# Optimization experiments

Measured on AMD Instinct MI355X. Metric: run time of the kernel, lower is better.

## Reference

```python
import jax, jax.numpy as jnp
import numpy as np
from functools import partial

MAX_SPAN_WIDTH = 8


def setup_inputs() -> dict:
    key = jax.random.key(0)
    ks = jax.random.split(key, 8)
    B, S, H = 4, 256, 256
    NE, D = 50000, 256  # entity_embedding_dim == hidden_size
    inp = {
        "embeddings": jax.random.normal(ks[0], (B, S, H), jnp.float32),          # BERT outputs[0]
        "entity_table": jax.random.normal(ks[1], (NE, D), jnp.float32) * 0.02,   # nn.Embedding weight
        "span_W": jax.random.normal(ks[2], (2 * H + 1, H), jnp.float32) * 0.02,  # span_embedding Linear
        "span_b": jax.random.normal(ks[3], (H,), jnp.float32) * 0.02,
        "gcn_W1": jax.random.normal(ks[4], (D, H), jnp.float32) * 0.02,
        "gcn_b1": jax.random.normal(ks[5], (H,), jnp.float32) * 0.02,
        "gcn_W2": jax.random.normal(ks[6], (H, H), jnp.float32) * 0.02,
        "gcn_b2": jax.random.normal(ks[7], (H,), jnp.float32) * 0.02,
        "k": 8,
    }
    return inp


def _star_adj_norm(k, dtype):
    # k-node star graph (node 0 hub) with self-loops, symmetric GCN normalization
    A = jnp.zeros((k, k), dtype).at[0, 1:].set(1.0).at[1:, 0].set(1.0) + jnp.eye(k, dtype=dtype)
    deg = A.sum(axis=1)
    return A / jnp.sqrt(deg[:, None] * deg[None, :])


def reference(embeddings, entity_table, span_W, span_b, gcn_W1, gcn_b1, gcn_W2, gcn_b2, k):
    B, S, H = embeddings.shape
    Wmax = MAX_SPAN_WIDTH
    dtype = embeddings.dtype

    # token_inputs: CLS embedding per example
    cls = embeddings[:, 0, :]  # [B, H]

    # Vectorized ragged span max-pool: running max over widths 1..Wmax.
    # span_max[w, b, s, :] = max(embeddings[b, s : s+w+1, :])
    neg_inf = jnp.array(-jnp.inf, dtype)
    maxes = []
    cur = embeddings
    maxes.append(cur)
    for w in range(1, Wmax):
        shifted = jnp.concatenate(
            [embeddings[:, w:, :], jnp.full((B, w, H), neg_inf, dtype)], axis=1)
        cur = jnp.maximum(cur, shifted)  # -inf pad => out-of-range positions ignored
        maxes.append(cur)
    span_max = jnp.stack(maxes, axis=0)  # [Wmax, B, S, H]

    # concat(max-pool, CLS, span width) -> span_embedding Linear
    cls_b = jnp.broadcast_to(cls[None, :, None, :], (Wmax, B, S, H))
    width_feat = jnp.broadcast_to(
        jnp.arange(1, Wmax + 1, dtype=dtype)[:, None, None, None], (Wmax, B, S, 1))
    span_inputs = jnp.concatenate([span_max, cls_b, width_feat], axis=-1)  # [Wmax,B,S,2H+1]
    span_inputs = span_inputs.reshape(Wmax * B * S, 2 * H + 1)             # [N, 2H+1]
    span_repr = span_inputs @ span_W + span_b                              # [N, H]

    # build_subgraph: top-k similar entities per span (memory-bound similarity + top-k)
    sims = span_repr @ entity_table.T          # [N, NE]  ~1.6GB intermediate
    _, topk_idx = jax.lax.top_k(sims, k)       # [N, k]
    node_x = entity_table[topk_idx]            # gather -> [N, k, D]

    # 2-layer GCN on the fixed star subgraph (gather-linear-scatter equivalent)
    A_norm = _star_adj_norm(k, dtype)          # [k, k]
    h = jax.nn.relu(jnp.einsum('ij,njd,dh->nih', A_norm, node_x, gcn_W1) + gcn_b1)
    subgraph_out = jnp.einsum('ij,njd,dh->nih', A_norm, h, gcn_W2) + gcn_b2  # [N, k, H]

    return cls, span_repr, subgraph_out
```

## Files before the change

### kernel.cpp

```cpp
#include <hip/hip_runtime.h>

typedef unsigned short u16;
typedef unsigned int   u32;
typedef unsigned long long u64;
typedef short bf16x8 __attribute__((ext_vector_type(8)));
typedef float f32x4  __attribute__((ext_vector_type(4)));

#define INF_F __builtin_inff()

__device__ __forceinline__ u16 f2bf(float f) {
  u32 u = __float_as_uint(f);
  return (u16)((u + 0x7FFFu + ((u >> 16) & 1u)) >> 16);
}

__device__ __forceinline__ u32 sortf(float f) {
  u32 u = __float_as_uint(f);
  return u ^ ((u32)((int)u >> 31) | 0x80000000u);
}
__device__ __forceinline__ float unsortf(u32 s) {
  u32 u = s ^ ((s & 0x80000000u) ? 0x80000000u : 0xFFFFFFFFu);
  return __uint_as_float(u);
}
__device__ __forceinline__ u64 sx64(u64 v, int m) {
  u32 lo = __shfl_xor((u32)v, m);
  u32 hi = __shfl_xor((u32)(v >> 32), m);
  return ((u64)hi << 32) | lo;
}

__global__ __launch_bounds__(256) void k0_cvt(
    const float* __restrict__ src, u16* __restrict__ dst, int n4) {
  int id = blockIdx.x * 256 + threadIdx.x;
  if (id >= n4) return;
  float4 v = ((const float4*)src)[id];
  ((ushort4*)dst)[id] = make_ushort4(f2bf(v.x), f2bf(v.y), f2bf(v.z), f2bf(v.w));
}

__global__ __launch_bounds__(256) void k1_span(
    const float* __restrict__ emb, const float* __restrict__ Wsp,
    const float* __restrict__ bsp,
    float* __restrict__ out0, float* __restrict__ out1,
    u16* __restrict__ spanbf) {
  __shared__ float SM[8][256];
  __shared__ float CLS[256];
  const int bid = blockIdx.x;
  const int b = bid >> 8, s = bid & 255;
  const int t = threadIdx.x;
  const float* eb = emb + (size_t)b * 65536;

  CLS[t] = eb[t];
  if (s == 0) out0[b * 256 + t] = eb[t];

  float m = eb[s * 256 + t];
  SM[0][t] = m;
  #pragma unroll
  for (int w = 1; w < 8; ++w) {
    if (s + w < 256) m = fmaxf(m, eb[(s + w) * 256 + t]);
    SM[w][t] = m;
  }
  __syncthreads();

  float cc = 0.f;
  for (int k = 0; k < 256; k += 4) {
    float4 cq = *(const float4*)&CLS[k];
    cc += cq.x * Wsp[(size_t)(256 + k + 0) * 256 + t];
    cc += cq.y * Wsp[(size_t)(256 + k + 1) * 256 + t];
    cc += cq.z * Wsp[(size_t)(256 + k + 2) * 256 + t];
    cc += cq.w * Wsp[(size_t)(256 + k + 3) * 256 + t];
  }
  float acc[8];
  const float base = bsp[t] + cc;
  #pragma unroll
  for (int w = 0; w < 8; ++w) acc[w] = base;

  for (int k = 0; k < 256; k += 4) {
    float w0 = Wsp[(size_t)(k + 0) * 256 + t];
    float w1 = Wsp[(size_t)(k + 1) * 256 + t];
    float w2 = Wsp[(size_t)(k + 2) * 256 + t];
    float w3 = Wsp[(size_t)(k + 3) * 256 + t];
    #pragma unroll
    for (int w = 0; w < 8; ++w) {
      float4 smq = *(const float4*)&SM[w][k];
      acc[w] += smq.x * w0; acc[w] += smq.y * w1;
      acc[w] += smq.z * w2; acc[w] += smq.w * w3;
    }
  }
  const float wm = Wsp[(size_t)512 * 256 + t];
  #pragma unroll
  for (int w = 0; w < 8; ++w) {
    float val = acc[w] + (float)(w + 1) * wm;
    size_t idx = ((size_t)w * 1024 + bid) * 256 + t;
    out1[idx] = val;
    spanbf[idx] = f2bf(val);
  }
}

__global__ __launch_bounds__(256) void k2_mfma(
    const u16* __restrict__ spanbf, const u16* __restrict__ entbf, int ne,
    float* __restrict__ Rpv, int* __restrict__ Rpi) {
  __shared__ u32 Elds[8192];
  __shared__ u64 Q[4][16][17];
  const int t = threadIdx.x, lane = t & 63, wv = t >> 6;
  const int m = lane & 15, q = lane >> 4, q4 = q * 4;
  const int rg = blockIdx.x & 63, p = blockIdx.x >> 6;
  const int psz = (ne + 7) >> 3;
  const int e_start = p * psz;
  const int e_end = min(ne, e_start + psz);
  const int rowbase = rg * 128 + wv * 32;
  const u64 gm = 0xFFFFull << (q * 16);
  const u64 lanelow = (lane == 63) ? 0x7FFFFFFFFFFFFFFFull
                                   : ((1ull << (lane + 1)) - 1) >> 1;
  const u64 gml = gm & lanelow;
  const int row = lane & 15;

  const u64 KINIT = ((u64)sortf(-INF_F) << 32);
  u64 slot0[4], slot1[4];
  #pragma unroll
  for (int s = 0; s < 4; ++s) { slot0[s] = KINIT; slot1[s] = KINIT; }
  float myth0 = -INF_F, myth1 = -INF_F;
  float th0[4], th1[4];
  #pragma unroll
  for (int r = 0; r < 4; ++r) { th0[r] = -INF_F; th1[r] = -INF_F; }

  bf16x8 a0[8], a1[8];
  #pragma unroll
  for (int s = 0; s < 8; ++s) {
    a0[s] = *(const bf16x8*)(spanbf + (size_t)(rowbase + m) * 256 + s * 32 + q * 8);
    a1[s] = *(const bf16x8*)(spanbf + (size_t)(rowbase + 16 + m) * 256 + s * 32 + q * 8);
  }

  uint4 stg[8];
  auto load_stage = [&](int tile) {
    const int ebs = e_start + (tile << 6);
    #pragma unroll
    for (int i = 0; i < 8; ++i) {
      int id = t + 256 * i; int e = id >> 5, qq = id & 31;
      int ge = ebs + e;
      uint4 v = make_uint4(0u, 0u, 0u, 0u);
      if (ge < e_end) v = *(const uint4*)((const char*)entbf + (size_t)ge * 512 + qq * 16);
      stg[i] = v;
    }
  };
  auto write_stage = [&]() {
    #pragma unroll
    for (int i = 0; i < 8; ++i) {
      int id = t + 256 * i; int e = id >> 5, qq = id & 31;
      *(uint4*)((char*)Elds + (((e << 5) | (qq ^ (e & 31))) << 4)) = stg[i];
    }
  };

  const int ntiles = (e_end - e_start + 63) >> 6;
  load_stage(0);

  for (int tile = 0; tile < ntiles; ++tile) {
    const int eb = e_start + (tile << 6);
    __syncthreads();
    write_stage();
    if (tile + 1 < ntiles) load_stage(tile + 1);
    __syncthreads();

    for (int c = 0; c < 4; ++c) {
      f32x4 acc0 = {0.f, 0.f, 0.f, 0.f}, acc1 = {0.f, 0.f, 0.f, 0.f};
      const int el = c * 16 + m, sw = el & 31, bc = el << 5;
      #pragma unroll
      for (int s = 0; s < 8; ++s) {
        int qq = s * 4 + q;
        bf16x8 bfr = *(const bf16x8*)((const char*)Elds + ((bc | (qq ^ sw)) << 4));
        acc0 = __builtin_amdgcn_mfma_f32_16x16x32_bf16(a0[s], bfr, acc0, 0, 0, 0);
        acc1 = __builtin_amdgcn_mfma_f32_16x16x32_bf16(a1[s], bfr, acc1, 0, 0, 0);
      }
      const int gent = eb + c * 16 + m;
      const bool valid = gent < e_end;

      auto produce = [&](const f32x4& av, const float* th, u64* M) {
        #pragma unroll
        for (int r = 0; r < 4; ++r) {
          bool hr = valid && (av[r] > th[r]);
          u64 br = __ballot(hr);
          M[r] = br;
          if (hr) {
            int pos = (int)__popcll(br & gml);
            Q[wv][q4 + r][pos] = ((u64)sortf(av[r]) << 32) | (u32)(~(u32)gent);
          }
        }
      };
      auto drain = [&](const u64* M, u64* slot, float& myth) {
        if (!(M[0] | M[1] | M[2] | M[3])) return;
        u64 msk = (row & 2) ? ((row & 1) ? M[3] : M[2])
                            : ((row & 1) ? M[1] : M[0]);
        int cnt = (int)__popcll((msk >> ((row >> 2) << 4)) & 0xFFFFull);
        int cmax = cnt;
        #pragma unroll
        for (int o = 1; o < 16; o <<= 1)
          cmax = max(cmax, __shfl_xor(cmax, o));
        for (int j = 0; j < cmax; ++j) {
          u64 cand = Q[wv][row][j];
          if (j >= cnt) cand = 0;
          u64 m01 = slot[0] < slot[1] ? slot[0] : slot[1];
          u64 m23 = slot[2] < slot[3] ? slot[2] : slot[3];
          u64 lmin = m01 < m23 ? m01 : m23;
          u64 g = sx64(lmin, 16); if (g < lmin) lmin = g;
          g = sx64(lmin, 32); u64 gmin = (g < lmin) ? g : lmin;
          bool ins = cand > gmin;
          #pragma unroll
          for (int s2 = 0; s2 < 4; ++s2)
            if (ins && slot[s2] == gmin) slot[s2] = cand;
        }
        u64 m01 = slot[0] < slot[1] ? slot[0] : slot[1];
        u64 m23 = slot[2] < slot[3] ? slot[2] : slot[3];
        u64 lmin = m01 < m23 ? m01 : m23;
        u64 g = sx64(lmin, 16); if (g < lmin) lmin = g;
        g = sx64(lmin, 32); if (g < lmin) lmin = g;
        myth = unsortf((u32)(lmin >> 32));
      };

      u64 M0[4], M1[4];
      produce(acc0, th0, M0);
      drain(M0, slot0, myth0);
      produce(acc1, th1, M1);
      drain(M1, slot1, myth1);
      if (M0[0] | M0[1] | M0[2] | M0[3]) {
        #pragma unroll
        for (int r = 0; r < 4; ++r) th0[r] = __shfl(myth0, q4 + r);
      }
      if (M1[0] | M1[1] | M1[2] | M1[3]) {
        #pragma unroll
        for (int r = 0; r < 4; ++r) th1[r] = __shfl(myth1, q4 + r);
      }
    }
  }

  {
    const int sg = lane >> 4;
    const int r0 = rowbase + row, r1 = rowbase + 16 + row;
    #pragma unroll
    for (int s = 0; s < 4; ++s) {
      u64 e0 = slot0[s], e1 = slot1[s];
      int col = p * 16 + sg * 4 + s;
      Rpv[(size_t)r0 * 128 + col] = unsortf((u32)(e0 >> 32));
      Rpi[(size_t)r0 * 128 + col] = (int)(~(u32)e0);
      Rpv[(size_t)r1 * 128 + col] = unsortf((u32)(e1 >> 32));
      Rpi[(size_t)r1 * 128 + col] = (int)(~(u32)e1);
    }
  }
}

__global__ __launch_bounds__(256) void k2_merge(
    const float* __restrict__ Rpv, const int* __restrict__ Rpi,
    int* __restrict__ Ridx) {
  const int t = threadIdx.x, lane = t & 63, wv = t >> 6;
  const int row = blockIdx.x * 4 + wv;
  const float va = Rpv[(size_t)row * 128 + lane];
  const int   ea = Rpi[(size_t)row * 128 + lane];
  const float vb = Rpv[(size_t)row * 128 + 64 + lane];
  const int   eb = Rpi[(size_t)row * 128 + 64 + lane];
  int ca = 0, cb = 0;
  for (int i = 0; i < 64; ++i) {
    float ov = __shfl(va, i); int oi = __shfl(ea, i);
    ca += (ov > va || (ov == va && oi < ea));
    cb += (ov > vb || (ov == vb && oi < eb));
  }
  for (int i = 0; i < 64; ++i) {
    float ov = __shfl(vb, i); int oi = __shfl(eb, i);
    ca += (ov > va || (ov == va && oi < ea));
    cb += (ov > vb || (ov == vb && oi < eb));
  }
  if (ca < 16) Ridx[(size_t)row * 16 + ca] = ea;
  if (cb < 16) Ridx[(size_t)row * 16 + cb] = eb;
}

__global__ __launch_bounds__(256, 3) void k3_gcn(
    const float* __restrict__ out1, const float* __restrict__ ent,
    const int* __restrict__ Ridx,
    const float* __restrict__ W1, const float* __restrict__ b1,
    const float* __restrict__ W2, const float* __restrict__ b2,
    float* __restrict__ out2, int ne) {
  __shared__ __align__(16) char UN[34560];
  __shared__ __align__(16) u16 Abf[32][272];
  __shared__ int cidx[4][16];
  __shared__ int chos[4][8];
  const int t = threadIdx.x;
  const int lane = t & 63, wv = t >> 6;
  const int m = lane & 15, q = lane >> 4;
  const int n0 = blockIdx.x * 4;

  {
    float  (*SPR)[256] = (float (*)[256])UN;
    double (*dpart)[4] = (double (*)[4])(UN + 4096);
    double (*sims)[16] = (double (*)[16])(UN + 6144);
    #pragma unroll
    for (int g = 0; g < 4; ++g)
      SPR[g][t] = out1[(size_t)(n0 + g) * 256 + t];
    if (t < 64) {
      int g = t >> 4, j = t & 15;
      int c = Ridx[(size_t)(n0 + g) * 16 + j];
      if ((unsigned)c >= (unsigned)ne) c = 0;
      cidx[g][j] = c;
    }
    __syncthreads();

    {
      const int pr = t >> 2, sub = t & 3;
      const int g = pr >> 4, j = pr & 15;
      const float* er = ent + (size_t)cidx[g][j] * 256 + sub * 64;
      const float* sr = &SPR[g][sub * 64];
      double s = 0.0;
      #pragma unroll
      for (int i = 0; i < 64; i += 4) {
        float4 e4 = *(const float4*)&er[i];
        float4 s4 = *(const float4*)&sr[i];
        s += (double)e4.x * (double)s4.x;
        s += (double)e4.y * (double)s4.y;
        s += (double)e4.z * (double)s4.z;
        s += (double)e4.w * (double)s4.w;
      }
      dpart[pr][sub] = s;
    }
    __syncthreads();
    if (t < 64) {
      int g = t >> 4, j = t & 15;
      sims[g][j] = dpart[t][0] + dpart[t][1] + dpart[t][2] + dpart[t][3];
    }
    __syncthreads();
    if (t < 4) {
      unsigned used = 0;
      for (int o = 0; o < 8; ++o) {
        int best = -1; double bv = 0.0; int bi = 0;
        for (int j = 0; j < 16; ++j) {
          if (used & (1u << j)) continue;
          if (best < 0 || sims[t][j] > bv || (sims[t][j] == bv && cidx[t][j] < bi)) {
            best = j; bv = sims[t][j]; bi = cidx[t][j];
          }
        }
        used |= (1u << best);
        chos[t][o] = cidx[t][best];
      }
    }
    __syncthreads();
  }

  {
    const int r = t >> 3, cb = t & 7;
    const float* src = ent + (size_t)chos[r >> 3][r & 7] * 256 + cb * 32;
    u32 pk[16];
    #pragma unroll
    for (int i = 0; i < 8; ++i) {
      float4 v = *(const float4*)&src[i * 4];
      pk[2 * i]     = (u32)f2bf(v.x) | ((u32)f2bf(v.y) << 16);
      pk[2 * i + 1] = (u32)f2bf(v.z) | ((u32)f2bf(v.w) << 16);
    }
    uint4* dst = (uint4*)&Abf[r][cb * 32];
    #pragma unroll
    for (int i = 0; i < 4; ++i)
      dst[i] = make_uint4(pk[4 * i], pk[4 * i + 1], pk[4 * i + 2], pk[4 * i + 3]);
  }

  auto run_gemm = [&](const float* __restrict__ Wg) {
    f32x4 acc[2][4];
    #pragma unroll
    for (int mt = 0; mt < 2; ++mt)
      #pragma unroll
      for (int nt = 0; nt < 4; ++nt)
        acc[mt][nt] = (f32x4){0.f, 0.f, 0.f, 0.f};

    for (int s = 0; s < 8; ++s) {
      __syncthreads();
      {
        const float* src = Wg + (size_t)(s * 32) * 256 + t;
        u32 pk[16];
        #pragma unroll
        for (int i = 0; i < 16; ++i) {
          float lo = src[(size_t)(2 * i) * 256];
          float hi = src[(size_t)(2 * i + 1) * 256];
          pk[i] = (u32)f2bf(lo) | ((u32)f2bf(hi) << 16);
        }
        uint4* dst = (uint4*)(UN + t * 80);
        #pragma unroll
        for (int i = 0; i < 4; ++i)
          dst[i] = make_uint4(pk[4 * i], pk[4 * i + 1], pk[4 * i + 2], pk[4 * i + 3]);
      }
      __syncthreads();
      #pragma unroll
      for (int mt = 0; mt < 2; ++mt) {
        bf16x8 af = *(const bf16x8*)((const char*)Abf
                       + (mt * 16 + m) * 544 + s * 64 + q * 16);
        #pragma unroll
        for (int nt = 0; nt < 4; ++nt) {
          const int col = wv * 64 + nt * 16 + m;
          bf16x8 bf = *(const bf16x8*)(UN + col * 80 + q * 16);
          acc[mt][nt] = __builtin_amdgcn_mfma_f32_16x16x32_bf16(
              af, bf, acc[mt][nt], 0, 0, 0);
        }
      }
    }
    __syncthreads();
    #pragma unroll
    for (int mt = 0; mt < 2; ++mt)
      #pragma unroll
      for (int nt = 0; nt < 4; ++nt)
        #pragma unroll
        for (int r = 0; r < 4; ++r)
          *(float*)(UN + (((mt * 16 + q * 4 + r) * 268)
                          + (wv * 64 + nt * 16 + m)) * 4) = acc[mt][nt][r];
    __syncthreads();
  };

  run_gemm(W1);
  {
    const float bb = b1[t];
    #pragma unroll
    for (int g = 0; g < 4; ++g) {
      float v[8];
      #pragma unroll
      for (int j = 0; j < 8; ++j)
        v[j] = *(const float*)(UN + ((g * 8 + j) * 268 + t) * 4);
      float ssum = 0.f;
      #pragma unroll
      for (int j = 1; j < 8; ++j) ssum += v[j];
      Abf[g * 8][t] = f2bf(fmaxf(v[0] * 0.125f + ssum * 0.25f + bb, 0.f));
      #pragma unroll
      for (int j = 1; j < 8; ++j)
        Abf[g * 8 + j][t] = f2bf(fmaxf(v[0] * 0.25f + v[j] * 0.5f + bb, 0.f));
    }
  }

  run_gemm(W2);
  {
    const float bb = b2[t];
    #pragma unroll
    for (int g = 0; g < 4; ++g) {
      float v[8];
      #pragma unroll
      for (int j = 0; j < 8; ++j)
        v[j] = *(const float*)(UN + ((g * 8 + j) * 268 + t) * 4);
      float ssum = 0.f;
      #pragma unroll
      for (int j = 1; j < 8; ++j) ssum += v[j];
      float* ob = out2 + (size_t)(n0 + g) * 2048 + t;
      ob[0] = v[0] * 0.125f + ssum * 0.25f + bb;
      #pragma unroll
      for (int j = 1; j < 8; ++j)
        ob[(size_t)j * 256] = v[0] * 0.25f + v[j] * 0.5f + bb;
    }
  }
}

extern "C" void kernel_launch(void* const* d_in, const int* in_sizes, int n_in,
                              void* d_out, int out_size, void* d_ws, size_t ws_size,
                              hipStream_t stream) {
  const float* emb = (const float*)d_in[0];
  const float* ent = (const float*)d_in[1];
  const float* Wsp = (const float*)d_in[2];
  const float* bsp = (const float*)d_in[3];
  const float* W1  = (const float*)d_in[4];
  const float* b1  = (const float*)d_in[5];
  const float* W2  = (const float*)d_in[6];
  const float* b2  = (const float*)d_in[7];
  const int ne = in_sizes[1] / 256;

  float* out  = (float*)d_out;
  float* out0 = out;
  float* out1 = out + 1024;
  float* out2 = out + 1024 + 2097152;

  char* ov = (char*)out2;
  u16*   entbf  = (u16*)(ov);
  u16*   spanbf = (u16*)(ov + 33554432);
  float* Rpv    = (float*)(ov + 41943040);
  int*   Rpi    = (int*)  (ov + 50331648);
  int*   Ridx   = (int*)d_ws;

  hipLaunchKernelGGL(k0_cvt, dim3((ne * 64 + 255) / 256), dim3(256), 0, stream,
                     ent, entbf, ne * 64);
  hipLaunchKernelGGL(k1_span, dim3(1024), dim3(256), 0, stream,
                     emb, Wsp, bsp, out0, out1, spanbf);
  hipLaunchKernelGGL(k2_mfma, dim3(512), dim3(256), 0, stream,
                     spanbf, entbf, ne, Rpv, Rpi);
  hipLaunchKernelGGL(k2_merge, dim3(2048), dim3(256), 0, stream,
                     Rpv, Rpi, Ridx);
  hipLaunchKernelGGL(k3_gcn, dim3(2048), dim3(256), 0, stream,
                     out1, ent, Ridx, W1, b1, W2, b2, out2, ne);
}
```

Measured before the change: 755.6 us.

## Use direct global-to-LDS loads with per-chunk pipelining and 64-row waves

```diff
diff --git a/kernel.cpp b/kernel.cpp
--- a/kernel.cpp
+++ b/kernel.cpp
@@ -25,6 +25,12 @@
   u32 lo = __shfl_xor((u32)v, m);
   u32 hi = __shfl_xor((u32)(v >> 32), m);
   return ((u64)hi << 32) | lo;
+}
+
+__device__ __forceinline__ void gload_lds16(const void* g, void* l) {
+  __builtin_amdgcn_global_load_lds(
+      (const __attribute__((address_space(1))) u32*)g,
+      (__attribute__((address_space(3))) u32*)l, 16, 0, 0);
 }
 
 __global__ __launch_bounds__(256) void k0_cvt(
@@ -94,97 +100,101 @@
   }
 }
 
-__global__ __launch_bounds__(256) void k2_mfma(
+__global__ __launch_bounds__(128) void k2_mfma(
     const u16* __restrict__ spanbf, const u16* __restrict__ entbf, int ne,
     float* __restrict__ Rpv, int* __restrict__ Rpi) {
   __shared__ u32 Elds[8192];
-  __shared__ u64 Q[4][16][17];
+  __shared__ u64 Q[2][64][17];
   const int t = threadIdx.x, lane = t & 63, wv = t >> 6;
   const int m = lane & 15, q = lane >> 4, q4 = q * 4;
-  const int rg = blockIdx.x & 63, p = blockIdx.x >> 6;
+  const int p = blockIdx.x & 7, rg = blockIdx.x >> 3;
   const int psz = (ne + 7) >> 3;
   const int e_start = p * psz;
   const int e_end = min(ne, e_start + psz);
-  const int rowbase = rg * 128 + wv * 32;
+  const int rowbase = rg * 128 + wv * 64;
   const u64 gm = 0xFFFFull << (q * 16);
   const u64 lanelow = (lane == 63) ? 0x7FFFFFFFFFFFFFFFull
                                    : ((1ull << (lane + 1)) - 1) >> 1;
   const u64 gml = gm & lanelow;
   const int row = lane & 15;
+  const int ls5 = lane >> 5;
 
   const u64 KINIT = ((u64)sortf(-INF_F) << 32);
-  u64 slot0[4], slot1[4];
-  #pragma unroll
-  for (int s = 0; s < 4; ++s) { slot0[s] = KINIT; slot1[s] = KINIT; }
-  float myth0 = -INF_F, myth1 = -INF_F;
-  float th0[4], th1[4];
-  #pragma unroll
-  for (int r = 0; r < 4; ++r) { th0[r] = -INF_F; th1[r] = -INF_F; }
-
-  bf16x8 a0[8], a1[8];
-  #pragma unroll
-  for (int s = 0; s < 8; ++s) {
-    a0[s] = *(const bf16x8*)(spanbf + (size_t)(rowbase + m) * 256 + s * 32 + q * 8);
-    a1[s] = *(const bf16x8*)(spanbf + (size_t)(rowbase + 16 + m) * 256 + s * 32 + q * 8);
-  }
-
-  uint4 stg[8];
-  auto load_stage = [&](int tile) {
-    const int ebs = e_start + (tile << 6);
-    #pragma unroll
-    for (int i = 0; i < 8; ++i) {
-      int id = t + 256 * i; int e = id >> 5, qq = id & 31;
-      int ge = ebs + e;
-      uint4 v = make_uint4(0u, 0u, 0u, 0u);
-      if (ge < e_end) v = *(const uint4*)((const char*)entbf + (size_t)ge * 512 + qq * 16);
-      stg[i] = v;
+  u64 slot[4][4];
+  float myth[4], th[4][4];
+  #pragma unroll
+  for (int h = 0; h < 4; ++h) {
+    myth[h] = -INF_F;
+    #pragma unroll
+    for (int s = 0; s < 4; ++s) { slot[h][s] = KINIT; th[h][s] = -INF_F; }
+  }
+
+  bf16x8 a[4][8];
+  #pragma unroll
+  for (int h = 0; h < 4; ++h)
+    #pragma unroll
+    for (int s = 0; s < 8; ++s)
+      a[h][s] = *(const bf16x8*)(spanbf
+                  + (size_t)(rowbase + h * 16 + m) * 256 + s * 32 + q * 8);
+
+  auto issue = [&](int c, int ebase) {
+    #pragma unroll
+    for (int i = 0; i < 4; ++i) {
+      int e = c * 16 + wv * 8 + i * 2 + ls5;
+      int ge = min(ebase + e, e_end - 1);
+      int xoff = ((lane & 31) ^ (e & 31)) << 4;
+      const char* src = (const char*)entbf + (size_t)ge * 512 + xoff;
+      char* dst = (char*)Elds + (c << 13) + (wv << 12) + (i << 10);
+      gload_lds16(src, dst);
     }
   };
-  auto write_stage = [&]() {
-    #pragma unroll
-    for (int i = 0; i < 8; ++i) {
-      int id = t + 256 * i; int e = id >> 5, qq = id & 31;
-      *(uint4*)((char*)Elds + (((e << 5) | (qq ^ (e & 31))) << 4)) = stg[i];
-    }
-  };
 
   const int ntiles = (e_end - e_start + 63) >> 6;
-  load_stage(0);
+  #pragma unroll
+  for (int c = 0; c < 4; ++c) issue(c, e_start);
 
   for (int tile = 0; tile < ntiles; ++tile) {
     const int eb = e_start + (tile << 6);
-    __syncthreads();
-    write_stage();
-    if (tile + 1 < ntiles) load_stage(tile + 1);
-    __syncthreads();
-
+    const int ebn = eb + 64;
+    const bool notlast = (tile + 1 < ntiles);
+    #pragma unroll
     for (int c = 0; c < 4; ++c) {
-      f32x4 acc0 = {0.f, 0.f, 0.f, 0.f}, acc1 = {0.f, 0.f, 0.f, 0.f};
+      if (notlast) asm volatile("s_waitcnt vmcnt(12)" ::: "memory");
+      else         asm volatile("s_waitcnt vmcnt(0)"  ::: "memory");
+      __builtin_amdgcn_sched_barrier(0);
+      __builtin_amdgcn_s_barrier();
+
+      f32x4 acc[4];
+      #pragma unroll
+      for (int h = 0; h < 4; ++h) acc[h] = (f32x4){0.f, 0.f, 0.f, 0.f};
       const int el = c * 16 + m, sw = el & 31, bc = el << 5;
       #pragma unroll
       for (int s = 0; s < 8; ++s) {
         int qq = s * 4 + q;
         bf16x8 bfr = *(const bf16x8*)((const char*)Elds + ((bc | (qq ^ sw)) << 4));
-        acc0 = __builtin_amdgcn_mfma_f32_16x16x32_bf16(a0[s], bfr, acc0, 0, 0, 0);
-        acc1 = __builtin_amdgcn_mfma_f32_16x16x32_bf16(a1[s], bfr, acc1, 0, 0, 0);
+        #pragma unroll
+        for (int h = 0; h < 4; ++h)
+          acc[h] = __builtin_amdgcn_mfma_f32_16x16x32_bf16(a[h][s], bfr, acc[h], 0, 0, 0);
       }
       const int gent = eb + c * 16 + m;
       const bool valid = gent < e_end;
 
-      auto produce = [&](const f32x4& av, const float* th, u64* M) {
+      #pragma unroll
+      for (int h = 0; h < 4; ++h) {
+        bool any = valid & ((acc[h][0] > th[h][0]) | (acc[h][1] > th[h][1]) |
+                            (acc[h][2] > th[h][2]) | (acc[h][3] > th[h][3]));
+        if (!__ballot(any)) continue;
+        u64 M[4];
         #pragma unroll
         for (int r = 0; r < 4; ++r) {
-          bool hr = valid && (av[r] > th[r]);
-          u64 br = __ballot(hr);
-          M[r] = br;
+          bool hr = valid && (acc[h][r] > th[h][r]);
+          M[r] = __ballot(hr);
           if (hr) {
-            int pos = (int)__popcll(br & gml);
-            Q[wv][q4 + r][pos] = ((u64)sortf(av[r]) << 32) | (u32)(~(u32)gent);
+            int pos = (int)__popcll(M[r] & gml);
+            Q[wv][h * 16 + q4 + r][pos] =
+                ((u64)sortf(acc[h][r]) << 32) | (u32)(~(u32)gent);
           }
         }
-      };
-      auto drain = [&](const u64* M, u64* slot, float& myth) {
-        if (!(M[0] | M[1] | M[2] | M[3])) return;
         u64 msk = (row & 2) ? ((row & 1) ? M[3] : M[2])
                             : ((row & 1) ? M[1] : M[0]);
         int cnt = (int)__popcll((msk >> ((row >> 2) << 4)) & 0xFFFFull);
@@ -193,53 +203,47 @@
         for (int o = 1; o < 16; o <<= 1)
           cmax = max(cmax, __shfl_xor(cmax, o));
         for (int j = 0; j < cmax; ++j) {
-          u64 cand = Q[wv][row][j];
+          u64 cand = Q[wv][h * 16 + row][j];
           if (j >= cnt) cand = 0;
-          u64 m01 = slot[0] < slot[1] ? slot[0] : slot[1];
-          u64 m23 = slot[2] < slot[3] ? slot[2] : slot[3];
+          u64 m01 = slot[h][0] < slot[h][1] ? slot[h][0] : slot[h][1];
+          u64 m23 = slot[h][2] < slot[h][3] ? slot[h][2] : slot[h][3];
           u64 lmin = m01 < m23 ? m01 : m23;
           u64 g = sx64(lmin, 16); if (g < lmin) lmin = g;
           g = sx64(lmin, 32); u64 gmin = (g < lmin) ? g : lmin;
           bool ins = cand > gmin;
           #pragma unroll
           for (int s2 = 0; s2 < 4; ++s2)
-            if (ins && slot[s2] == gmin) slot[s2] = cand;
-        }
-        u64 m01 = slot[0] < slot[1] ? slot[0] : slot[1];
-        u64 m23 = slot[2] < slot[3] ? slot[2] : slot[3];
-        u64 lmin = m01 < m23 ? m01 : m23;
-        u64 g = sx64(lmin, 16); if (g < lmin) lmin = g;
-        g = sx64(lmin, 32); if (g < lmin) lmin = g;
-        myth = unsortf((u32)(lmin >> 32));
-      };
-
-      u64 M0[4], M1[4];
-      produce(acc0, th0, M0);
-      drain(M0, slot0, myth0);
-      produce(acc1, th1, M1);
-      drain(M1, slot1, myth1);
-      if (M0[0] | M0[1] | M0[2] | M0[3]) {
-        #pragma unroll
-        for (int r = 0; r < 4; ++r) th0[r] = __shfl(myth0, q4 + r);
-      }
-      if (M1[0] | M1[1] | M1[2] | M1[3]) {
-        #pragma unroll
-        for (int r = 0; r < 4; ++r) th1[r] = __shfl(myth1, q4 + r);
-      }
+            if (ins && slot[h][s2] == gmin) slot[h][s2] = cand;
+        }
+        {
+          u64 m01 = slot[h][0] < slot[h][1] ? slot[h][0] : slot[h][1];
+          u64 m23 = slot[h][2] < slot[h][3] ? slot[h][2] : slot[h][3];
+          u64 lmin = m01 < m23 ? m01 : m23;
+          u64 g = sx64(lmin, 16); if (g < lmin) lmin = g;
+          g = sx64(lmin, 32); if (g < lmin) lmin = g;
+          myth[h] = unsortf((u32)(lmin >> 32));
+          #pragma unroll
+          for (int r = 0; r < 4; ++r) th[h][r] = __shfl(myth[h], q4 + r);
+        }
+      }
+
+      __builtin_amdgcn_s_barrier();
+      if (notlast) issue(c, ebn);
     }
   }
 
   {
     const int sg = lane >> 4;
-    const int r0 = rowbase + row, r1 = rowbase + 16 + row;
-    #pragma unroll
-    for (int s = 0; s < 4; ++s) {
-      u64 e0 = slot0[s], e1 = slot1[s];
-      int col = p * 16 + sg * 4 + s;
-      Rpv[(size_t)r0 * 128 + col] = unsortf((u32)(e0 >> 32));
-      Rpi[(size_t)r0 * 128 + col] = (int)(~(u32)e0);
-      Rpv[(size_t)r1 * 128 + col] = unsortf((u32)(e1 >> 32));
-      Rpi[(size_t)r1 * 128 + col] = (int)(~(u32)e1);
+    #pragma unroll
+    for (int h = 0; h < 4; ++h) {
+      int r0 = rowbase + h * 16 + row;
+      #pragma unroll
+      for (int s = 0; s < 4; ++s) {
+        u64 e0 = slot[h][s];
+        int col = p * 16 + sg * 4 + s;
+        Rpv[(size_t)r0 * 128 + col] = unsortf((u32)(e0 >> 32));
+        Rpi[(size_t)r0 * 128 + col] = (int)(~(u32)e0);
+      }
     }
   }
 }
@@ -473,7 +477,7 @@
                      ent, entbf, ne * 64);
   hipLaunchKernelGGL(k1_span, dim3(1024), dim3(256), 0, stream,
                      emb, Wsp, bsp, out0, out1, spanbf);
-  hipLaunchKernelGGL(k2_mfma, dim3(512), dim3(256), 0, stream,
+  hipLaunchKernelGGL(k2_mfma, dim3(512), dim3(128), 0, stream,
                      spanbf, entbf, ne, Rpv, Rpi);
   hipLaunchKernelGGL(k2_merge, dim3(2048), dim3(256), 0, stream,
                      Rpv, Rpi, Ridx);
```

Measured after the change: 883.1 us. 1.17x slower.
